# Performance work log

Measured on AMD Instinct MI355X. Metric: run time of the kernel, lower is better.

Reference implementation:

```python
import jax, jax.numpy as jnp
import numpy as np

T, N, E = 4, 50000, 800000
F, H, C_HID, C_OUT = 256, 128, 512, 2
SLOPE = 11.0 / 48.0  # torch RReLU eval-mode slope = (1/8 + 1/3) / 2


def _topk_pool(x, scorer, k):
    # x: [N, d], scorer: [d, 1] -> [d, k]
    scores = (x @ scorer) / jnp.maximum(jnp.linalg.norm(scorer), 1e-6)  # [N, 1]
    _, idx = jax.lax.top_k(scores[:, 0], k)
    return (x[idx] * jnp.tanh(scores[idx])).T


def _gru_cell(prev_Q, z, Wu, Uu, bu, Wr, Ur, br, Wh, Uh, bh):
    u = jax.nn.sigmoid(Wu @ z + Uu @ prev_Q + bu)
    r = jax.nn.sigmoid(Wr @ z + Ur @ prev_Q + br)
    h_cap = jnp.tanh(Wh @ z + Uh @ (r * prev_Q) + bh)
    return (1.0 - u) * prev_Q + u * h_cap


def _gcn_conv(x, src, dst, W):
    ones = jnp.ones(src.shape[0], x.dtype)
    deg_out = jnp.clip(jax.ops.segment_sum(ones, src, num_segments=N), 1.0)
    deg_in = jnp.clip(jax.ops.segment_sum(ones, dst, num_segments=N), 1.0)
    h = (x * (deg_out ** -0.5)[:, None]) @ W          # project first (out <= in)
    agg = jax.ops.segment_sum(h[src], dst, num_segments=N)
    out = agg * (deg_in ** -0.5)[:, None]
    return jnp.where(out >= 0, out, SLOPE * out)      # RReLU (eval mode)


def setup_inputs() -> dict:
    key = jax.random.key(0)
    ks = jax.random.split(key, 32)
    s = 0.05
    d = {}
    d['feats'] = jax.random.normal(ks[0], (T, N, F), jnp.float32)
    d['edges'] = jax.random.randint(ks[1], (T, 2, E), 0, N)
    d['scorer0'] = jax.random.normal(ks[2], (F, 1), jnp.float32) * s
    d['scorer1'] = jax.random.normal(ks[3], (H, 1), jnp.float32) * s
    d['gcn_W0'] = jax.random.normal(ks[4], (F, H), jnp.float32) * s
    d['gcn_W1'] = jax.random.normal(ks[5], (H, H), jnp.float32) * s
    i = 6
    for g in ('u', 'r', 'h'):
        d[g + '_W0'] = jax.random.normal(ks[i], (F, F), jnp.float32) * s; i += 1
        d[g + '_U0'] = jax.random.normal(ks[i], (F, F), jnp.float32) * s; i += 1
        d[g + '_b0'] = jax.random.normal(ks[i], (F, H), jnp.float32) * s; i += 1
    for g in ('u', 'r', 'h'):
        d[g + '_W1'] = jax.random.normal(ks[i], (H, H), jnp.float32) * s; i += 1
        d[g + '_U1'] = jax.random.normal(ks[i], (H, H), jnp.float32) * s; i += 1
        d[g + '_b1'] = jax.random.normal(ks[i], (H, H), jnp.float32) * s; i += 1
    d['mlp_W1'] = jax.random.normal(ks[i], (H, C_HID), jnp.float32) * s; i += 1
    d['mlp_b1'] = jax.random.normal(ks[i], (C_HID,), jnp.float32) * s; i += 1
    d['mlp_W2'] = jax.random.normal(ks[i], (C_HID, C_OUT), jnp.float32) * s; i += 1
    d['mlp_b2'] = jax.random.normal(ks[i], (C_OUT,), jnp.float32) * s
    return d


def reference(feats, edges, scorer0, scorer1, gcn_W0, gcn_W1,
              u_W0, u_U0, u_b0, r_W0, r_U0, r_b0, h_W0, h_U0, h_b0,
              u_W1, u_U1, u_b1, r_W1, r_U1, r_b1, h_W1, h_U1, h_b1,
              mlp_W1, mlp_b1, mlp_W2, mlp_b2):
    feat_list = [feats[t] for t in range(T)]
    scorers = [scorer0, scorer1]
    gcn_Ws = [gcn_W0, gcn_W1]
    grus = [(u_W0, u_U0, u_b0, r_W0, r_U0, r_b0, h_W0, h_U0, h_b0),
            (u_W1, u_U1, u_b1, r_W1, r_U1, r_b1, h_W1, h_U1, h_b1)]
    for i in range(2):
        W = gcn_Ws[i]
        for t in range(T):
            src, dst = edges[t, 0], edges[t, 1]
            X_tilde = _topk_pool(feat_list[t], scorers[i], H)
            W = _gru_cell(W, X_tilde, *grus[i])
            feat_list[t] = _gcn_conv(feat_list[t], src, dst, W)
    x = feat_list[-1]
    x = jnp.maximum(x @ mlp_W1 + mlp_b1, 0.0)
    return x @ mlp_W2 + mlp_b2
```

## Files before the change

### kernel.cpp

```cpp
#include <hip/hip_runtime.h>

#define NT 4
#define NN 50000
#define NE 800000
#define FD 256
#define HD 128
#define CH 512
#define NBINS 4096
#define CAPC 256
#define RSLOPE 0.22916666666666666f

#define NCH 32
#define CHE (NE / NCH)
#define HALFN 25000
#define WPH 12500
#define WPC 25000

#define C_NORM0 0
#define C_NORM1 1

#define SCAN_BLOCKS 49
#define BT0SZ (HD * 2 * FD)
#define BT1SZ (HD * 2 * HD)

#define SU_NORM0 0
#define SU_NORM1 1
#define SU_CVT_A 2
#define SU_CVT_B 66
#define SU_CVT_C 98
#define SU_CAT0 114
#define SU_CAT1 1650
#define SU_SPL0 2034
#define SU_SPL1 2290
#define SU_CPQ0 2354
#define SU_CPQ1 2386
#define SU_ZBAR 2402
#define SU_TOTAL 2403

typedef __attribute__((ext_vector_type(8))) short bf16x8;
typedef __attribute__((ext_vector_type(4))) float f32x4;

__device__ __forceinline__ float wsumf(float v) {
  for (int m = 32; m > 0; m >>= 1) v += __shfl_xor(v, m, 64);
  return v;
}

__device__ __forceinline__ unsigned short f2bf(float x) {
  unsigned int u = __float_as_uint(x);
  u += 0x7fffu + ((u >> 16) & 1u);
  return (unsigned short)(u >> 16);
}
__device__ __forceinline__ float bf2f(unsigned short h) {
  return __uint_as_float(((unsigned int)h) << 16);
}
__device__ __forceinline__ int sbin(float s) {
  int b = (int)floorf((s + 16.f) * 128.f);
  return max(0, min(NBINS - 1, b));
}

__device__ __forceinline__ void gbar(unsigned int* bar, int nblk, int gen) {
  __syncthreads();
  if (threadIdx.x == 0) {
    __threadfence();
    atomicAdd(bar, 1u);
    unsigned int tgt = (unsigned int)(nblk * (gen + 1));
    while (atomicAdd(bar, 0u) < tgt) __builtin_amdgcn_s_sleep(2);
    __threadfence();
  }
  __syncthreads();
}

__device__ __forceinline__ void d_norm(const float* s, int d, float* ctlf, int slot,
                                       float* red) {
  float v = ((int)threadIdx.x < d) ? s[threadIdx.x] * s[threadIdx.x] : 0.f;
  red[threadIdx.x] = v;
  __syncthreads();
  for (int o = 128; o > 0; o >>= 1) {
    if ((int)threadIdx.x < o) red[threadIdx.x] += red[threadIdx.x + o];
    __syncthreads();
  }
  if (threadIdx.x == 0) ctlf[slot] = fmaxf(sqrtf(red[0]), 1e-6f);
}

__device__ __forceinline__ void d_cvtT(int bx, int by, const float* __restrict__ src, int C,
                                       unsigned short* __restrict__ dhi,
                                       unsigned short* __restrict__ dlo,
                                       int ldd, int roff, float (*t)[33]) {
  int bc = bx * 32, br = by * 32;
  int lr = threadIdx.x >> 5, lc = threadIdx.x & 31;
#pragma unroll
  for (int q = 0; q < 4; ++q) {
    int r = br + lr + q * 8;
    t[lr + q * 8][lc] = src[(size_t)r * C + bc + lc];
  }
  __syncthreads();
#pragma unroll
  for (int q = 0; q < 4; ++q) {
    int dr = lr + q * 8;
    float v = t[lc][dr];
    unsigned short h = f2bf(v);
    unsigned short l = f2bf(v - bf2f(h));
    size_t o = (size_t)(bc + dr) * ldd + roff + br + lc;
    dhi[o] = h;
    dlo[o] = l;
  }
}

__device__ __forceinline__ void d_catsplit(int blk, int d, const float* __restrict__ Wu,
                                           const float* __restrict__ Uu,
                                           const float* __restrict__ Wr,
                                           const float* __restrict__ Ur,
                                           const float* __restrict__ Wh,
                                           unsigned short* __restrict__ hi,
                                           unsigned short* __restrict__ lo) {
  int idx = blk * 256 + threadIdx.x;
  int K = 2 * d;
  if (idx >= 3 * d * K) return;
  int row = idx / K, col = idx - row * K;
  int reg = row / d;
  int i = row - reg * d;
  float v;
  if (reg == 0) v = (col < d) ? Wu[i * d + col] : Uu[i * d + col - d];
  else if (reg == 1) v = (col < d) ? Wr[i * d + col] : Ur[i * d + col - d];
  else v = (col < d) ? Wh[i * d + col] : 0.f;
  unsigned short h = f2bf(v);
  hi[idx] = h;
  lo[idx] = f2bf(v - bf2f(h));
}

__device__ __forceinline__ void d_split(int blk, int n, const float* __restrict__ src,
                                        unsigned short* __restrict__ hi,
                                        unsigned short* __restrict__ lo) {
  int idx = blk * 256 + threadIdx.x;
  if (idx >= n) return;
  float v = src[idx];
  unsigned short h = f2bf(v);
  hi[idx] = h;
  lo[idx] = f2bf(v - bf2f(h));
}

__global__ __launch_bounds__(256) void k_startup(
    const float* __restrict__ scorer0, const float* __restrict__ scorer1,
    float* __restrict__ ctlf,
    const float* __restrict__ mlpW1, unsigned short* __restrict__ mW1thi,
    unsigned short* __restrict__ mW1tlo,
    const float* __restrict__ gcnW0, const float* __restrict__ gcnW1,
    unsigned short* __restrict__ bt0hi, unsigned short* __restrict__ bt0lo,
    unsigned short* __restrict__ bt1hi, unsigned short* __restrict__ bt1lo,
    const float* __restrict__ u_W0, const float* __restrict__ u_U0,
    const float* __restrict__ r_W0, const float* __restrict__ r_U0,
    const float* __restrict__ h_W0,
    unsigned short* __restrict__ acat0hi, unsigned short* __restrict__ acat0lo,
    const float* __restrict__ u_W1, const float* __restrict__ u_U1,
    const float* __restrict__ r_W1, const float* __restrict__ r_U1,
    const float* __restrict__ h_W1,
    unsigned short* __restrict__ acat1hi, unsigned short* __restrict__ acat1lo,
    const float* __restrict__ uh0, unsigned short* __restrict__ uh0hi,
    unsigned short* __restrict__ uh0lo,
    const float* __restrict__ uh1, unsigned short* __restrict__ uh1hi,
    unsigned short* __restrict__ uh1lo,
    float* __restrict__ Q0, float* __restrict__ Q1,
    unsigned int* __restrict__ bar) {
  __shared__ float red[256];
  __shared__ float tile[32][33];
  int b = blockIdx.x;
  if (b == SU_NORM0) { d_norm(scorer0, FD, ctlf, C_NORM0, red); return; }
  if (b == SU_NORM1) { d_norm(scorer1, HD, ctlf, C_NORM1, red); return; }
  if (b < SU_CVT_B) { int r = b - SU_CVT_A; d_cvtT(r & 15, r >> 4, mlpW1, CH, mW1thi, mW1tlo, HD, 0, tile); return; }
  if (b < SU_CVT_C) { int r = b - SU_CVT_B; d_cvtT(r & 3, r >> 2, gcnW0, HD, bt0hi, bt0lo, 2 * FD, FD, tile); return; }
  if (b < SU_CAT0)  { int r = b - SU_CVT_C; d_cvtT(r & 3, r >> 2, gcnW1, HD, bt1hi, bt1lo, 2 * HD, HD, tile); return; }
  if (b < SU_CAT1)  { d_catsplit(b - SU_CAT0, FD, u_W0, u_U0, r_W0, r_U0, h_W0, acat0hi, acat0lo); return; }
  if (b < SU_SPL0)  { d_catsplit(b - SU_CAT1, HD, u_W1, u_U1, r_W1, r_U1, h_W1, acat1hi, acat1lo); return; }
  if (b < SU_SPL1)  { d_split(b - SU_SPL0, FD * FD, uh0, uh0hi, uh0lo); return; }
  if (b < SU_CPQ0)  { d_split(b - SU_SPL1, HD * HD, uh1, uh1hi, uh1lo); return; }
  if (b < SU_CPQ1)  { int i = (b - SU_CPQ0) * 256 + threadIdx.x; ((float4*)Q0)[i] = ((const float4*)gcnW0)[i]; return; }
  if (b < SU_ZBAR)  { int i = (b - SU_CPQ1) * 256 + threadIdx.x; ((float4*)Q1)[i] = ((const float4*)gcnW1)[i]; return; }
  if (threadIdx.x < 16) bar[threadIdx.x] = 0;
}

__global__ __launch_bounds__(1024) void k_degC(const int* __restrict__ edges,
                                               unsigned int* __restrict__ chist) {
  __shared__ unsigned int lcnt[WPH];
  int t = blockIdx.y, c = blockIdx.x;
  int tid = threadIdx.x;
  for (int dir = 0; dir < 2; ++dir) {
    const int* E = edges + (size_t)t * 2 * NE + (size_t)dir * NE + (size_t)c * CHE;
    for (int half = 0; half < 2; ++half) {
      for (int i = tid; i < WPH; i += 1024) lcnt[i] = 0;
      __syncthreads();
      int lo = half * HALFN;
      for (int j = tid; j < CHE; j += 1024) {
        int n = E[j] - lo;
        if ((unsigned)n < (unsigned)HALFN)
          atomicAdd(&lcnt[n >> 1], 1u << ((n & 1) * 16));
      }
      __syncthreads();
      unsigned int* dst = chist + (((size_t)dir * NT + t) * NCH + c) * WPC + (size_t)half * WPH;
      for (int i = tid; i < WPH; i += 1024) dst[i] = lcnt[i];
      __syncthreads();
    }
  }
}

__global__ __launch_bounds__(1024) void k_scanB(const unsigned int* __restrict__ chist,
                                                unsigned int* __restrict__ lbase,
                                                float* __restrict__ dor4,
                                                float* __restrict__ din4,
                                                int* __restrict__ rowptr4,
                                                int* __restrict__ bsum4) {
  int t = blockIdx.y;
  int tid = threadIdx.x;
  int g = blockIdx.x * 1024 + tid;
  int lane = tid & 63, wid = tid >> 6;
  int v = 0;
  if (g < NN) {
    int w = g >> 1, sh = (g & 1) * 16;
    const unsigned int* oh = chist + ((size_t)0 * NT + t) * NCH * WPC;
    const unsigned int* ih = chist + ((size_t)1 * NT + t) * NCH * WPC;
    int o = 0;
#pragma unroll
    for (int c = 0; c < NCH; ++c) o += (oh[(size_t)c * WPC + w] >> sh) & 0xffff;
    dor4[t * NN + g] = 1.f / sqrtf((float)max(o, 1));
    int run = 0;
#pragma unroll
    for (int c = 0; c < NCH; ++c) {
      lbase[((size_t)t * NCH + c) * NN + g] = (unsigned int)run;
      run += (ih[(size_t)c * WPC + w] >> sh) & 0xffff;
    }
    v = run;
    din4[t * NN + g] = 1.f / sqrtf((float)max(v, 1));
  }
  int s = v;
  for (int o = 1; o < 64; o <<= 1) {
    int u = __shfl_up(s, o, 64);
    if (lane >= o) s += u;
  }
  __shared__ int ws[16];
  if (lane == 63) ws[wid] = s;
  __syncthreads();
  if (wid == 0 && lane < 16) {
    int u = ws[lane];
    int ss = u;
    for (int o = 1; o < 16; o <<= 1) {
      int w2 = __shfl_up(ss, o, 64);
      if (lane >= o) ss += w2;
    }
    ws[lane] = ss - u;
  }
  __syncthreads();
  int incl = s + ws[wid];
  if (g < NN) rowptr4[(size_t)t * (NN + 1) + g] = incl - v;
  if (tid == 1023) bsum4[t * SCAN_BLOCKS + blockIdx.x] = incl;
}

__global__ __launch_bounds__(1024) void k_scan2b(int* __restrict__ rowptr4,
                                                 const int* __restrict__ bsum4) {
  int t = blockIdx.x;
  int* rowptr = rowptr4 + (size_t)t * (NN + 1);
  const int* bsum = bsum4 + t * SCAN_BLOCKS;
  __shared__ int boff[SCAN_BLOCKS];
// ... 77 lines not shown
  __shared__ float stv[HD];
  __shared__ int sidx[HD];
  __shared__ int thrBin, cnt;
  int tid = threadIdx.x;
  for (int i = tid; i < NBINS; i += 1024) hist[i] = 0;
  if (tid == 0) cnt = 0;
  __syncthreads();
  for (int i = tid; i < NN; i += 1024) atomicAdd(&hist[sbin(scores[i])], 1);
  __syncthreads();

  int h0 = hist[4 * tid + 0], h1 = hist[4 * tid + 1];
  int h2 = hist[4 * tid + 2], h3 = hist[4 * tid + 3];
  int l3 = h3, l2 = h2 + l3, l1 = h1 + l2, l0 = h0 + l1;
  sufT[tid] = l0;
  __syncthreads();
  for (int off = 1; off < 1024; off <<= 1) {
    int u = (tid + off < 1024) ? sufT[tid + off] : 0;
    __syncthreads();
    sufT[tid] += u;
    __syncthreads();
  }
  {
    int higher = sufT[tid] - l0;
    int S0 = l0 + higher, S1 = l1 + higher, S2 = l2 + higher, S3 = l3 + higher;
    int S4 = higher;
    if (S3 >= HD && S4 < HD) thrBin = 4 * tid + 3;
    else if (S2 >= HD && S3 < HD) thrBin = 4 * tid + 2;
    else if (S1 >= HD && S2 < HD) thrBin = 4 * tid + 1;
    else if (S0 >= HD && S1 < HD) thrBin = 4 * tid + 0;
  }
  __syncthreads();
  int thr = thrBin;
  for (int i = tid; i < NN; i += 1024) {
    float s = scores[i];
    if (sbin(s) >= thr) {
      int p = atomicAdd(&cnt, 1);
      if (p < CAPC) { cs[p] = s; ci[p] = i; }
    }
  }
  __syncthreads();
  int M = min(cnt, CAPC);
  for (int i = tid; i < CAPC; i += 1024)
    if (i >= M) { cs[i] = -3.4e38f; ci[i] = 0x7fffffff; }
  __syncthreads();
  for (int k = 2; k <= CAPC; k <<= 1) {
    for (int j = k >> 1; j > 0; j >>= 1) {
      int i = tid;
      if (i < CAPC) {
        int l = i ^ j;
        if (l > i) {
          float si = cs[i], sl = cs[l];
          int di = ci[i], dl = ci[l];
          bool lb = (sl > si) || (sl == si && dl < di);
          bool ib = (si > sl) || (si == sl && di < dl);
          bool dir = ((i & k) == 0);
          if (dir ? lb : ib) {
            cs[i] = sl; cs[l] = si; ci[i] = dl; ci[l] = di;
          }
        }
      }
      __syncthreads();
    }
  }
  if (tid < HD) {
    stv[tid] = tanhf(cs[tid]);
    sidx[tid] = ci[tid];
  }
  __syncthreads();
  for (int e4 = tid * 4; e4 < D * HD; e4 += 1024 * 4) {
    int j = e4 >> LOGD, f = e4 & (D - 1);
    float4 x = *(const float4*)&X[(size_t)sidx[j] * D + f];
    float sv = stv[j];
    x.x *= sv; x.y *= sv; x.z *= sv; x.w *= sv;
    ushort4 h, l;
    h.x = f2bf(x.x); l.x = f2bf(x.x - bf2f(h.x));
    h.y = f2bf(x.y); l.y = f2bf(x.y - bf2f(h.y));
    h.z = f2bf(x.z); l.z = f2bf(x.z - bf2f(h.z));
    h.w = f2bf(x.w); l.w = f2bf(x.w - bf2f(h.w));
    *(ushort4*)&bthi[(size_t)j * ldb + f] = h;
    *(ushort4*)&btlo[(size_t)j * ldb + f] = l;
  }
}

__device__ __forceinline__ void gruA_body(
    int bx, const unsigned short* __restrict__ Ahi, const unsigned short* __restrict__ Alo,
    const unsigned short* __restrict__ Bhi, const unsigned short* __restrict__ Blo,
    int d, const float* __restrict__ bu, const float* __restrict__ br,
    const float* __restrict__ bh, const float* __restrict__ Q,
    float* __restrict__ u, float* __restrict__ hz,
    unsigned short* __restrict__ rqThi, unsigned short* __restrict__ rqTlo,
    unsigned short* AshH, unsigned short* AshL,
    unsigned short* BshH, unsigned short* BshL) {
  int K = 2 * d;
  int tid = threadIdx.x;
  int lane = tid & 63, wave = tid >> 6;
  int wr = wave >> 1, wc = wave & 1;
  int n0 = bx * 64;
  f32x4 acc[2][4];
#pragma unroll
  for (int m = 0; m < 2; ++m)
#pragma unroll
    for (int n = 0; n < 4; ++n) acc[m][n] = (f32x4){0.f, 0.f, 0.f, 0.f};
  int arow = tid >> 2, aseg = tid & 3;
  int as = (aseg ^ (arow & 3)) * 8;
  int kseg = lane >> 4;
  for (int k0 = 0; k0 < K; k0 += 32) {
    __syncthreads();
    {
      size_t off = (size_t)(n0 + arow) * K + k0 + aseg * 8;
      *(bf16x8*)&AshH[arow * 32 + as] = *(const bf16x8*)(Ahi + off);
      *(bf16x8*)&AshL[arow * 32 + as] = *(const bf16x8*)(Alo + off);
    }
#pragma unroll
    for (int h = 0; h < 2; ++h) {
      int id = tid + h * 256;
      int br2 = id >> 2, bseg = id & 3;
      int bs = (bseg ^ (br2 & 3)) * 8;
      size_t off = (size_t)br2 * K + k0 + bseg * 8;
      *(bf16x8*)&BshH[br2 * 32 + bs] = *(const bf16x8*)(Bhi + off);
      *(bf16x8*)&BshL[br2 * 32 + bs] = *(const bf16x8*)(Blo + off);
    }
    __syncthreads();
    bf16x8 ah[2], al[2], bh8[4], bl8[4];
#pragma unroll
    for (int m = 0; m < 2; ++m) {
      int row = wr * 32 + m * 16 + (lane & 15);
      int s = (kseg ^ (row & 3)) * 8;
      ah[m] = *(bf16x8*)&AshH[row * 32 + s];
      al[m] = *(bf16x8*)&AshL[row * 32 + s];
    }
#pragma unroll
    for (int n = 0; n < 4; ++n) {
      int col = wc * 64 + n * 16 + (lane & 15);
      int s = (kseg ^ (col & 3)) * 8;
      bh8[n] = *(bf16x8*)&BshH[col * 32 + s];
      bl8[n] = *(bf16x8*)&BshL[col * 32 + s];
    }
#pragma unroll
    for (int m = 0; m < 2; ++m)
#pragma unroll
      for (int n = 0; n < 4; ++n) {
        acc[m][n] = __builtin_amdgcn_mfma_f32_16x16x32_bf16(ah[m], bh8[n], acc[m][n], 0, 0, 0);
        acc[m][n] = __builtin_amdgcn_mfma_f32_16x16x32_bf16(al[m], bh8[n], acc[m][n], 0, 0, 0);
        acc[m][n] = __builtin_amdgcn_mfma_f32_16x16x32_bf16(ah[m], bl8[n], acc[m][n], 0, 0, 0);
      }
  }
  int reg = n0 / d;
#pragma unroll
  for (int m = 0; m < 2; ++m) {
#pragma unroll
    for (int q = 0; q < 4; ++q) {
      int row = n0 + wr * 32 + m * 16 + (lane >> 4) * 4 + q;
      int i = row - reg * d;
#pragma unroll
      for (int n = 0; n < 4; ++n) {
        int col = wc * 64 + n * 16 + (lane & 15);
        float a = acc[m][n][q];
        if (reg == 0) {
          u[i * HD + col] = 1.f / (1.f + expf(-(a + bu[i * HD + col])));
        } else if (reg == 1) {
          float r = 1.f / (1.f + expf(-(a + br[i * HD + col])));
          float rq = r * Q[i * HD + col];
          unsigned short h = f2bf(rq);
          rqThi[(size_t)col * d + i] = h;
          rqTlo[(size_t)col * d + i] = f2bf(rq - bf2f(h));
        } else {
          hz[i * HD + col] = a + bh[i * HD + col];
        }
      }
    }
  }
}

__device__ __forceinline__ void gruB_body(
    int bx, const unsigned short* __restrict__ Ahi, const unsigned short* __restrict__ Alo,
    const unsigned short* __restrict__ Bhi, const unsigned short* __restrict__ Blo,
    int d, const float* __restrict__ hz, const float* __restrict__ u,
    float* __restrict__ Q, unsigned short* __restrict__ BTWhi,
    unsigned short* __restrict__ BTWlo, int ldbt,
    unsigned short* AshH, unsigned short* AshL,
    unsigned short* BshH, unsigned short* BshL) {
  int K = d;
  int tid = threadIdx.x;
  int lane = tid & 63, wave = tid >> 6;
  int wr = wave >> 1, wc = wave & 1;
  int n0 = bx * 64;
  f32x4 acc[2][4];
#pragma unroll
  for (int m = 0; m < 2; ++m)
#pragma unroll
    for (int n = 0; n < 4; ++n) acc[m][n] = (f32x4){0.f, 0.f, 0.f, 0.f};
  int arow = tid >> 2, aseg = tid & 3;
  int as = (aseg ^ (arow & 3)) * 8;
  int kseg = lane >> 4;
  for (int k0 = 0; k0 < K; k0 += 32) {
    __syncthreads();
    {
      size_t off = (size_t)(n0 + arow) * K + k0 + aseg * 8;
      *(bf16x8*)&AshH[arow * 32 + as] = *(const bf16x8*)(Ahi + off);
      *(bf16x8*)&AshL[arow * 32 + as] = *(const bf16x8*)(Alo + off);
    }
#pragma unroll
    for (int h = 0; h < 2; ++h) {
      int id = tid + h * 256;
      int br2 = id >> 2, bseg = id & 3;
      int bs = (bseg ^ (br2 & 3)) * 8;
      size_t off = (size_t)br2 * K + k0 + bseg * 8;
      *(bf16x8*)&BshH[br2 * 32 + bs] = *(const bf16x8*)(Bhi + off);
      *(bf16x8*)&BshL[br2 * 32 + bs] = *(const bf16x8*)(Blo + off);
    }
    __syncthreads();
    bf16x8 ah[2], al[2], bh8[4], bl8[4];
#pragma unroll
    for (int m = 0; m < 2; ++m) {
      int row = wr * 32 + m * 16 + (lane & 15);
      int s = (kseg ^ (row & 3)) * 8;
      ah[m] = *(bf16x8*)&AshH[row * 32 + s];
      al[m] = *(bf16x8*)&AshL[row * 32 + s];
    }
#pragma unroll
    for (int n = 0; n < 4; ++n) {
      int col = wc * 64 + n * 16 + (lane & 15);
      int s = (kseg ^ (col & 3)) * 8;
      bh8[n] = *(bf16x8*)&BshH[col * 32 + s];
      bl8[n] = *(bf16x8*)&BshL[col * 32 + s];
    }
#pragma unroll
    for (int m = 0; m < 2; ++m)
#pragma unroll
      for (int n = 0; n < 4; ++n) {
        acc[m][n] = __builtin_amdgcn_mfma_f32_16x16x32_bf16(ah[m], bh8[n], acc[m][n], 0, 0, 0);
        acc[m][n] = __builtin_amdgcn_mfma_f32_16x16x32_bf16(al[m], bh8[n], acc[m][n], 0, 0, 0);
        acc[m][n] = __builtin_amdgcn_mfma_f32_16x16x32_bf16(ah[m], bl8[n], acc[m][n], 0, 0, 0);
      }
  }
#pragma unroll
  for (int m = 0; m < 2; ++m) {
#pragma unroll
    for (int q = 0; q < 4; ++q) {
      int i = n0 + wr * 32 + m * 16 + (lane >> 4) * 4 + q;
#pragma unroll
      for (int n = 0; n < 4; ++n) {
        int col = wc * 64 + n * 16 + (lane & 15);
        float hc = tanhf(acc[m][n][q] + hz[i * HD + col]);
        float uu = u[i * HD + col];
        float qv = Q[i * HD + col];
        float wn = (1.f - uu) * qv + uu * hc;
        Q[i * HD + col] = wn;
        unsigned short h = f2bf(wn);
        BTWhi[(size_t)col * ldbt + i] = h;
        BTWlo[(size_t)col * ldbt + i] = f2bf(wn - bf2f(h));
      }
    }
  }
}

__global__ __launch_bounds__(256) void k_gruChain(
    const unsigned short* __restrict__ Ahi, const unsigned short* __restrict__ Alo,
    unsigned short* __restrict__ bthi, unsigned short* __restrict__ btlo, long btSz,
    int d, const float* __restrict__ gb_u, const float* __restrict__ gb_r,
    const float* __restrict__ gb_h, float* __restrict__ Q,
    float* __restrict__ ubuf, float* __restrict__ hzbuf,
    unsigned short* __restrict__ rqThi, unsigned short* __restrict__ rqTlo,
    const unsigned short* __restrict__ uhhi, const unsigned short* __restrict__ uhlo,
    unsigned int* bar) {
  __shared__ unsigned short AshH[64 * 32], AshL[64 * 32];
  __shared__ unsigned short BshH[128 * 32], BshL[128 * 32];
  int nb = (int)gridDim.x;
  for (int t = 0; t < NT; ++t) {
    gruA_body((int)blockIdx.x, Ahi, Alo,
              bthi + (size_t)t * btSz, btlo + (size_t)t * btSz, d,
              gb_u, gb_r, gb_h, Q, ubuf, hzbuf, rqThi, rqTlo,
              AshH, AshL, BshH, BshL);
    gbar(bar, nb, 2 * t);
    if ((int)blockIdx.x < (d >> 6)) {
      size_t nxt = (size_t)((t + 1) & 3) * btSz;
      gruB_body((int)blockIdx.x, uhhi, uhlo, rqThi, rqTlo, d, hzbuf, ubuf, Q,
                bthi + nxt + d, btlo + nxt + d, 2 * d,
                AshH, AshL, BshH, BshL);
    }
    if (t < NT - 1) gbar(bar, nb, 2 * t + 1);
  }
}

__global__ __launch_bounds__(256) void k_convL0(
    const float* __restrict__ feats,
    const unsigned short* __restrict__ bt0hi, const unsigned short* __restrict__ bt0lo,
    float* __restrict__ C4, const float* __restrict__ dor4) {
  __shared__ unsigned short AshH[64 * 32], AshL[64 * 32];
  __shared__ unsigned short BshH[128 * 32], BshL[128 * 32];
  const int K = FD, ldb = 2 * FD;
  int t = blockIdx.z;
  const float* Af = feats + (size_t)t * NN * FD;
  size_t bOff = (size_t)((t + 1) & 3) * BT0SZ + FD;
  const unsigned short* Bhi = bt0hi + bOff;
  const unsigned short* Blo = bt0lo + bOff;
  float* C = C4 + (size_t)t * NN * HD;
  const float* rs = dor4 + (size_t)t * NN;
  int tid = threadIdx.x;
  int lane = tid & 63, wave = tid >> 6;
  int wr = wave >> 1, wc = wave & 1;
  int n0 = blockIdx.x * 64;
  f32x4 acc[2][4];
#pragma unroll
  for (int m = 0; m < 2; ++m)
#pragma unroll
    for (int n = 0; n < 4; ++n) acc[m][n] = (f32x4){0.f, 0.f, 0.f, 0.f};

  int arow = tid >> 2, aseg = tid & 3;
  int as = (aseg ^ (arow & 3)) * 8;
  int kseg = lane >> 4;

  for (int k0 = 0; k0 < K; k0 += 32) {
    __syncthreads();
    {
      bf16x8 vh = (bf16x8)(short)0, vl = (bf16x8)(short)0;
      int row = n0 + arow;
      if (row < NN) {
        const float* g = Af + (size_t)row * K + k0 + aseg * 8;
        float4 v0 = *(const float4*)g;
        float4 v1 = *(const float4*)(g + 4);
        float xs[8] = {v0.x, v0.y, v0.z, v0.w, v1.x, v1.y, v1.z, v1.w};
#pragma unroll
        for (int j = 0; j < 8; ++j) {
          unsigned short h = f2bf(xs[j]);
          vh[j] = (short)h;
          vl[j] = (short)f2bf(xs[j] - bf2f(h));
        }
      }
      *(bf16x8*)&AshH[arow * 32 + as] = vh;
      *(bf16x8*)&AshL[arow * 32 + as] = vl;
    }
#pragma unroll
    for (int h = 0; h < 2; ++h) {
      int id = tid + h * 256;
      int br = id >> 2, bseg = id & 3;
      int bs = (bseg ^ (br & 3)) * 8;
      size_t off = (size_t)br * ldb + k0 + bseg * 8;
      *(bf16x8*)&BshH[br * 32 + bs] = *(const bf16x8*)(Bhi + off);
      *(bf16x8*)&BshL[br * 32 + bs] = *(const bf16x8*)(Blo + off);
    }
    __syncthreads();

    bf16x8 ah[2], al[2], bh[4], bl[4];
#pragma unroll
    for (int m = 0; m < 2; ++m) {
      int row = wr * 32 + m * 16 + (lane & 15);
      int s = (kseg ^ (row & 3)) * 8;
      ah[m] = *(bf16x8*)&AshH[row * 32 + s];
      al[m] = *(bf16x8*)&AshL[row * 32 + s];
    }
#pragma unroll
    for (int n = 0; n < 4; ++n) {
      int col = wc * 64 + n * 16 + (lane & 15);
      int s = (kseg ^ (col & 3)) * 8;
      bh[n] = *(bf16x8*)&BshH[col * 32 + s];
      bl[n] = *(bf16x8*)&BshL[col * 32 + s];
    }
#pragma unroll
    for (int m = 0; m < 2; ++m)
#pragma unroll
      for (int n = 0; n < 4; ++n) {
        acc[m][n] = __builtin_amdgcn_mfma_f32_16x16x32_bf16(ah[m], bh[n], acc[m][n], 0, 0, 0);
        acc[m][n] = __builtin_amdgcn_mfma_f32_16x16x32_bf16(al[m], bh[n], acc[m][n], 0, 0, 0);
// ... 174 lines not shown
#pragma unroll
    for (int m = 0; m < 2; ++m)
#pragma unroll
      for (int n = 0; n < 4; ++n) acc[m][n] = (f32x4){0.f, 0.f, 0.f, 0.f};
    for (int k0 = 0; k0 < HD; k0 += 32) {
      __syncthreads();
#pragma unroll
      for (int h2 = 0; h2 < 2; ++h2) {
        int id = tid + h2 * 256;
        int br = id >> 2, bseg = id & 3;
        int bs = (bseg ^ (br & 3)) * 8;
        size_t off = (size_t)(hc * 128 + br) * HD + k0 + bseg * 8;
        *(bf16x8*)&BshH[br * 32 + bs] = *(const bf16x8*)(Bhi + off);
        *(bf16x8*)&BshL[br * 32 + bs] = *(const bf16x8*)(Blo + off);
      }
      __syncthreads();
      bf16x8 ah[2], al[2], bh[4], bl[4];
#pragma unroll
      for (int m = 0; m < 2; ++m) {
        int row = wr * 32 + m * 16 + (lane & 15);
        int sg = (k0 >> 3) + kseg;
        int sp = (sg ^ (row & 15)) * 8;
        ah[m] = *(bf16x8*)&AshH[row * 128 + sp];
        al[m] = *(bf16x8*)&AshL[row * 128 + sp];
      }
#pragma unroll
      for (int n = 0; n < 4; ++n) {
        int col = wc * 64 + n * 16 + (lane & 15);
        int s = (kseg ^ (col & 3)) * 8;
        bh[n] = *(bf16x8*)&BshH[col * 32 + s];
        bl[n] = *(bf16x8*)&BshL[col * 32 + s];
      }
#pragma unroll
      for (int m = 0; m < 2; ++m)
#pragma unroll
        for (int n = 0; n < 4; ++n) {
          acc[m][n] = __builtin_amdgcn_mfma_f32_16x16x32_bf16(ah[m], bh[n], acc[m][n], 0, 0, 0);
          acc[m][n] = __builtin_amdgcn_mfma_f32_16x16x32_bf16(al[m], bh[n], acc[m][n], 0, 0, 0);
          acc[m][n] = __builtin_amdgcn_mfma_f32_16x16x32_bf16(ah[m], bl[n], acc[m][n], 0, 0, 0);
        }
    }
#pragma unroll
    for (int n = 0; n < 4; ++n) {
      int col = hc * 128 + wc * 64 + n * 16 + (lane & 15);
      float bcol = bias[col];
      float w20 = W2[2 * col], w21 = W2[2 * col + 1];
#pragma unroll
      for (int m = 0; m < 2; ++m)
#pragma unroll
        for (int q = 0; q < 4; ++q) {
          float v = fmaxf(acc[m][n][q] + bcol, 0.f);
          ps0[m][q] += v * w20;
          ps1[m][q] += v * w21;
        }
    }
  }
#pragma unroll
  for (int m = 0; m < 2; ++m)
#pragma unroll
    for (int q = 0; q < 4; ++q) {
      float a = ps0[m][q], b = ps1[m][q];
      for (int msk = 8; msk > 0; msk >>= 1) {
        a += __shfl_xor(a, msk, 64);
        b += __shfl_xor(b, msk, 64);
      }
      if ((lane & 15) == 0) {
        int r = wr * 32 + m * 16 + (lane >> 4) * 4 + q;
        atomicAdd(&osum[r][0], a);
        atomicAdd(&osum[r][1], b);
      }
    }
  __syncthreads();
  if (tid < 64) {
    int row = n0 + tid;
    if (row < M) {
      out[(size_t)row * 2 + 0] = osum[tid][0] + b2[0];
      out[(size_t)row * 2 + 1] = osum[tid][1] + b2[1];
    }
  }
}

__global__ void k_aggB(const float* __restrict__ h4, const int* __restrict__ rowptr4,
                       const int* __restrict__ srcs4, const float* __restrict__ din4,
                       float* __restrict__ featA4, const float* __restrict__ scorer,
                       const float* __restrict__ ctlf, float* __restrict__ scores1_4,
                       unsigned short* __restrict__ outHi, unsigned short* __restrict__ outLo) {
  int t = blockIdx.y;
  int w = (blockIdx.x * blockDim.x + threadIdx.x) >> 6;
  int lane = threadIdx.x & 63;
  if (w >= NN) return;
  const float* h = h4 + (size_t)t * NN * HD;
  const int* rowptr = rowptr4 + (size_t)t * (NN + 1);
  const int* srcs = srcs4 + (size_t)t * NE;
  int beg = rowptr[w], end = rowptr[w + 1];
  float ax = 0.f, ay = 0.f;
  int e = beg;
  int l2o = lane * 2;
  for (; e + 8 <= end; e += 8) {
    int s0 = srcs[e + 0], s1 = srcs[e + 1], s2 = srcs[e + 2], s3 = srcs[e + 3];
    int s4 = srcs[e + 4], s5 = srcs[e + 5], s6 = srcs[e + 6], s7 = srcs[e + 7];
    float2 v0 = *(const float2*)&h[(size_t)s0 * HD + l2o];
    float2 v1 = *(const float2*)&h[(size_t)s1 * HD + l2o];
    float2 v2 = *(const float2*)&h[(size_t)s2 * HD + l2o];
    float2 v3 = *(const float2*)&h[(size_t)s3 * HD + l2o];
    float2 v4 = *(const float2*)&h[(size_t)s4 * HD + l2o];
    float2 v5 = *(const float2*)&h[(size_t)s5 * HD + l2o];
    float2 v6 = *(const float2*)&h[(size_t)s6 * HD + l2o];
    float2 v7 = *(const float2*)&h[(size_t)s7 * HD + l2o];
    ax += ((v0.x + v1.x) + (v2.x + v3.x)) + ((v4.x + v5.x) + (v6.x + v7.x));
    ay += ((v0.y + v1.y) + (v2.y + v3.y)) + ((v4.y + v5.y) + (v6.y + v7.y));
  }
  for (; e + 2 <= end; e += 2) {
    int s0 = srcs[e + 0], s1 = srcs[e + 1];
    float2 v0 = *(const float2*)&h[(size_t)s0 * HD + l2o];
    float2 v1 = *(const float2*)&h[(size_t)s1 * HD + l2o];
    ax += v0.x + v1.x;
    ay += v0.y + v1.y;
  }
  for (; e < end; ++e) {
    int s = srcs[e];
    float2 v = *(const float2*)&h[(size_t)s * HD + l2o];
    ax += v.x; ay += v.y;
  }
  float dn = din4[(size_t)t * NN + w];
  ax *= dn; ay *= dn;
  ax = ax >= 0.f ? ax : RSLOPE * ax;
  ay = ay >= 0.f ? ay : RSLOPE * ay;
  *(float2*)&featA4[((size_t)t * NN + w) * HD + l2o] = make_float2(ax, ay);
  if (t == NT - 1) {
    unsigned short hx = f2bf(ax), hy = f2bf(ay);
    unsigned short lx = f2bf(ax - bf2f(hx)), ly = f2bf(ay - bf2f(hy));
    *(ushort2*)&outHi[(size_t)w * HD + l2o] = make_ushort2(hx, hy);
    *(ushort2*)&outLo[(size_t)w * HD + l2o] = make_ushort2(lx, ly);
  }
  float sp = ax * scorer[l2o] + ay * scorer[l2o + 1];
  sp = wsumf(sp);
  if (lane == 0) scores1_4[(size_t)t * NN + w] = sp / ctlf[C_NORM1];
}

extern "C" void kernel_launch(void* const* d_in, const int* in_sizes, int n_in,
                              void* d_out, int out_size, void* d_ws, size_t ws_size,
                              hipStream_t stream) {
  (void)in_sizes; (void)n_in; (void)out_size; (void)ws_size;
  const float* feats = (const float*)d_in[0];
  const int* edges = (const int*)d_in[1];
  const float* scorer0 = (const float*)d_in[2];
  const float* scorer1 = (const float*)d_in[3];
  const float* gcnW0 = (const float*)d_in[4];
  const float* gcnW1 = (const float*)d_in[5];
  const float* g0[9];
  const float* g1[9];
  for (int i = 0; i < 9; ++i) {
    g0[i] = (const float*)d_in[6 + i];
    g1[i] = (const float*)d_in[15 + i];
  }
  const float* mlpW1 = (const float*)d_in[24];
  const float* mlpB1 = (const float*)d_in[25];
  const float* mlpW2 = (const float*)d_in[26];
  const float* mlpB2 = (const float*)d_in[27];
  float* out = (float*)d_out;

  char* p = (char*)d_ws;
  auto carve = [&p](size_t bytes) {
    void* r = (void*)p;
    p += (bytes + 511) & ~(size_t)511;
    return r;
  };
  float* featA4 = (float*)carve((size_t)NT * NN * HD * 4);
  float* hbuf4  = (float*)carve((size_t)NT * NN * HD * 4);
  unsigned short* fahi = (unsigned short*)carve((size_t)NN * HD * 2);
  unsigned short* falo = (unsigned short*)carve((size_t)NN * HD * 2);
  int* srcs4   = (int*)carve((size_t)NT * NE * 4);
  int* rowptr4 = (int*)carve((size_t)NT * (NN + 1) * 4);
  unsigned int* chist = (unsigned int*)carve((size_t)2 * NT * NCH * WPC * 4);
  unsigned int* lbase = (unsigned int*)carve((size_t)NT * NCH * NN * 4);
  int* bsum4   = (int*)carve((size_t)NT * SCAN_BLOCKS * 4);
  float* dor4  = (float*)carve((size_t)NT * NN * 4);
  float* din4  = (float*)carve((size_t)NT * NN * 4);
  float* scores0 = (float*)carve((size_t)NT * NN * 4);
  float* scores1_4 = (float*)carve((size_t)NT * NN * 4);
  float* ctlf  = (float*)carve(64 * 4);
  unsigned short* bt0hi = (unsigned short*)carve((size_t)NT * BT0SZ * 2);
  unsigned short* bt0lo = (unsigned short*)carve((size_t)NT * BT0SZ * 2);
  unsigned short* bt1hi = (unsigned short*)carve((size_t)NT * BT1SZ * 2);
  unsigned short* bt1lo = (unsigned short*)carve((size_t)NT * BT1SZ * 2);
  unsigned short* rqThi = (unsigned short*)carve((size_t)HD * FD * 2);
  unsigned short* rqTlo = (unsigned short*)carve((size_t)HD * FD * 2);
  float* ubuf_f = (float*)carve((size_t)FD * HD * 4);
  float* hzbuf  = (float*)carve((size_t)FD * HD * 4);
  unsigned short* acat0hi = (unsigned short*)carve((size_t)3 * FD * 2 * FD * 2);
  unsigned short* acat0lo = (unsigned short*)carve((size_t)3 * FD * 2 * FD * 2);
  unsigned short* acat1hi = (unsigned short*)carve((size_t)3 * HD * 2 * HD * 2);
  unsigned short* acat1lo = (unsigned short*)carve((size_t)3 * HD * 2 * HD * 2);
  unsigned short* uh0hi = (unsigned short*)carve((size_t)FD * FD * 2);
  unsigned short* uh0lo = (unsigned short*)carve((size_t)FD * FD * 2);
  unsigned short* uh1hi = (unsigned short*)carve((size_t)HD * HD * 2);
  unsigned short* uh1lo = (unsigned short*)carve((size_t)HD * HD * 2);
  float* Q0 = (float*)carve((size_t)FD * HD * 4);
  float* Q1 = (float*)carve((size_t)HD * HD * 4);
  unsigned short* mW1thi = (unsigned short*)carve((size_t)CH * HD * 2);
  unsigned short* mW1tlo = (unsigned short*)carve((size_t)CH * HD * 2);
  unsigned int* barbuf = (unsigned int*)carve(64 * 4);

  k_startup<<<SU_TOTAL, 256, 0, stream>>>(
      scorer0, scorer1, ctlf, mlpW1, mW1thi, mW1tlo, gcnW0, gcnW1,
      bt0hi, bt0lo, bt1hi, bt1lo,
      g0[0], g0[1], g0[3], g0[4], g0[6], acat0hi, acat0lo,
      g1[0], g1[1], g1[3], g1[4], g1[6], acat1hi, acat1lo,
      g0[7], uh0hi, uh0lo, g1[7], uh1hi, uh1lo, Q0, Q1, barbuf);

  k_scores0_all<<<dim3(12500, NT), 256, 0, stream>>>(feats, scorer0, ctlf, scores0);
  k_degC<<<dim3(NCH, NT), 1024, 0, stream>>>(edges, chist);
  k_scanB<<<dim3(SCAN_BLOCKS, NT), 1024, 0, stream>>>(chist, lbase, dor4, din4, rowptr4, bsum4);
  k_scan2b<<<NT, 1024, 0, stream>>>(rowptr4, bsum4);
  k_scatC<<<dim3(NCH, NT), 1024, 0, stream>>>(edges, rowptr4, lbase, srcs4);
  k_pool<8><<<NT, 1024, 0, stream>>>(feats, (long)NN * FD, scores0, NN,
                                     bt0hi, bt0lo, (long)BT0SZ, 2 * FD);

  k_gruChain<<<3 * FD / 64, 256, 0, stream>>>(
      acat0hi, acat0lo, bt0hi, bt0lo, (long)BT0SZ, FD,
      g0[2], g0[5], g0[8], Q0, ubuf_f, hzbuf, rqThi, rqTlo,
      uh0hi, uh0lo, barbuf + 0);

  const int gM = (NN + 63) / 64;

  k_convL0<<<dim3(gM, 1, NT), 256, 0, stream>>>(feats, bt0hi, bt0lo, hbuf4, dor4);

  k_aggB<<<dim3(12500, NT), 256, 0, stream>>>(hbuf4, rowptr4, srcs4, din4, featA4,
                                              scorer1, ctlf, scores1_4, fahi, falo);

  k_pool<7><<<NT, 1024, 0, stream>>>(featA4, (long)NN * HD, scores1_4, NN,
                                     bt1hi, bt1lo, (long)BT1SZ, 2 * HD);

  k_gruChain<<<3 * HD / 64, 256, 0, stream>>>(
      acat1hi, acat1lo, bt1hi, bt1lo, (long)BT1SZ, HD,
      g1[2], g1[5], g1[8], Q1, ubuf_f, hzbuf, rqThi, rqTlo,
      uh1hi, uh1lo, barbuf + 1);

  k_gemm3<<<dim3(gM, 1), 256, 0, stream>>>(fahi, falo, HD,
                                           bt1hi + HD, bt1lo + HD, 2 * HD,
                                           hbuf4, HD, NN, HD, dor4 + (size_t)3 * NN);
  k_gemmMLPagg<<<gM, 256, 0, stream>>>(hbuf4, rowptr4 + (size_t)3 * (NN + 1),
                                       srcs4 + (size_t)3 * NE, din4 + (size_t)3 * NN,
                                       mW1thi, mW1tlo, mlpB1, mlpW2, mlpB2, out, NN);
}
```

Measured before the change: 1.126 ms.

## Drop featA buffer by recomputing pooled rows; split GRU chain into per-step launches

The layer-1 aggregation no longer writes the full fp32 featA tensor (4x50000x128). A new pool kernel instead recomputes aggregation, normalization and RReLU only for the 128 selected top-k nodes, directly from hbuf and the CSR. The persistent GRU chain kernel with its spin-wait grid barriers is replaced by separate gruA/gruB launches for each timestep. This removes a large write and reread of intermediate data and the barrier spinning, at the cost of 16 extra kernel launches and some redundant gather work in the pool kernel.

```diff
diff --git a/kernel.cpp b/kernel.cpp
--- a/kernel.cpp
+++ b/kernel.cpp
@@ -34,8 +34,7 @@
 #define SU_SPL1 2290
 #define SU_CPQ0 2354
 #define SU_CPQ1 2386
-#define SU_ZBAR 2402
-#define SU_TOTAL 2403
+#define SU_TOTAL 2402
 
 typedef __attribute__((ext_vector_type(8))) short bf16x8;
 typedef __attribute__((ext_vector_type(4))) float f32x4;
@@ -56,18 +55,6 @@
 __device__ __forceinline__ int sbin(float s) {
   int b = (int)floorf((s + 16.f) * 128.f);
   return max(0, min(NBINS - 1, b));
-}
-
-__device__ __forceinline__ void gbar(unsigned int* bar, int nblk, int gen) {
-  __syncthreads();
-  if (threadIdx.x == 0) {
-    __threadfence();
-    atomicAdd(bar, 1u);
-    unsigned int tgt = (unsigned int)(nblk * (gen + 1));
-    while (atomicAdd(bar, 0u) < tgt) __builtin_amdgcn_s_sleep(2);
-    __threadfence();
-  }
-  __syncthreads();
 }
 
 __device__ __forceinline__ void d_norm(const float* s, int d, float* ctlf, int slot,
@@ -159,8 +146,7 @@
     unsigned short* __restrict__ uh0lo,
     const float* __restrict__ uh1, unsigned short* __restrict__ uh1hi,
     unsigned short* __restrict__ uh1lo,
-    float* __restrict__ Q0, float* __restrict__ Q1,
-    unsigned int* __restrict__ bar) {
+    float* __restrict__ Q0, float* __restrict__ Q1) {
   __shared__ float red[256];
   __shared__ float tile[32][33];
   int b = blockIdx.x;
@@ -174,8 +160,7 @@
   if (b < SU_SPL1)  { d_split(b - SU_SPL0, FD * FD, uh0, uh0hi, uh0lo); return; }
   if (b < SU_CPQ0)  { d_split(b - SU_SPL1, HD * HD, uh1, uh1hi, uh1lo); return; }
   if (b < SU_CPQ1)  { int i = (b - SU_CPQ0) * 256 + threadIdx.x; ((float4*)Q0)[i] = ((const float4*)gcnW0)[i]; return; }
-  if (b < SU_ZBAR)  { int i = (b - SU_CPQ1) * 256 + threadIdx.x; ((float4*)Q1)[i] = ((const float4*)gcnW1)[i]; return; }
-  if (threadIdx.x < 16) bar[threadIdx.x] = 0;
+  { int i = (b - SU_CPQ1) * 256 + threadIdx.x; ((float4*)Q1)[i] = ((const float4*)gcnW1)[i]; }
 }
 
 __global__ __launch_bounds__(1024) void k_degC(const int* __restrict__ edges,
@@ -419,20 +404,20 @@
   }
 }
 
-__device__ __forceinline__ void gruA_body(
-    int bx, const unsigned short* __restrict__ Ahi, const unsigned short* __restrict__ Alo,
+__global__ __launch_bounds__(256) void k_gruA(
+    const unsigned short* __restrict__ Ahi, const unsigned short* __restrict__ Alo,
     const unsigned short* __restrict__ Bhi, const unsigned short* __restrict__ Blo,
     int d, const float* __restrict__ bu, const float* __restrict__ br,
     const float* __restrict__ bh, const float* __restrict__ Q,
     float* __restrict__ u, float* __restrict__ hz,
-    unsigned short* __restrict__ rqThi, unsigned short* __restrict__ rqTlo,
-    unsigned short* AshH, unsigned short* AshL,
-    unsigned short* BshH, unsigned short* BshL) {
+    unsigned short* __restrict__ rqThi, unsigned short* __restrict__ rqTlo) {
+  __shared__ unsigned short AshH[64 * 32], AshL[64 * 32];
+  __shared__ unsigned short BshH[128 * 32], BshL[128 * 32];
   int K = 2 * d;
   int tid = threadIdx.x;
   int lane = tid & 63, wave = tid >> 6;
   int wr = wave >> 1, wc = wave & 1;
-  int n0 = bx * 64;
+  int n0 = blockIdx.x * 64;
   f32x4 acc[2][4];
 #pragma unroll
   for (int m = 0; m < 2; ++m)
@@ -509,19 +494,19 @@
   }
 }
 
-__device__ __forceinline__ void gruB_body(
-    int bx, const unsigned short* __restrict__ Ahi, const unsigned short* __restrict__ Alo,
+__global__ __launch_bounds__(256) void k_gruB(
+    const unsigned short* __restrict__ Ahi, const unsigned short* __restrict__ Alo,
     const unsigned short* __restrict__ Bhi, const unsigned short* __restrict__ Blo,
     int d, const float* __restrict__ hz, const float* __restrict__ u,
     float* __restrict__ Q, unsigned short* __restrict__ BTWhi,
-    unsigned short* __restrict__ BTWlo, int ldbt,
-    unsigned short* AshH, unsigned short* AshL,
-    unsigned short* BshH, unsigned short* BshL) {
+    unsigned short* __restrict__ BTWlo, int ldbt) {
+  __shared__ unsigned short AshH[64 * 32], AshL[64 * 32];
+  __shared__ unsigned short BshH[128 * 32], BshL[128 * 32];
   int K = d;
   int tid = threadIdx.x;
   int lane = tid & 63, wave = tid >> 6;
   int wr = wave >> 1, wc = wave & 1;
-  int n0 = bx * 64;
+  int n0 = blockIdx.x * 64;
   f32x4 acc[2][4];
 #pragma unroll
   for (int m = 0; m < 2; ++m)
@@ -589,34 +574,6 @@
         BTWlo[(size_t)col * ldbt + i] = f2bf(wn - bf2f(h));
       }
     }
-  }
-}
-
-__global__ __launch_bounds__(256) void k_gruChain(
-    const unsigned short* __restrict__ Ahi, const unsigned short* __restrict__ Alo,
-    unsigned short* __restrict__ bthi, unsigned short* __restrict__ btlo, long btSz,
-    int d, const float* __restrict__ gb_u, const float* __restrict__ gb_r,
-    const float* __restrict__ gb_h, float* __restrict__ Q,
-    float* __restrict__ ubuf, float* __restrict__ hzbuf,
-    unsigned short* __restrict__ rqThi, unsigned short* __restrict__ rqTlo,
-    const unsigned short* __restrict__ uhhi, const unsigned short* __restrict__ uhlo,
-    unsigned int* bar) {
-  __shared__ unsigned short AshH[64 * 32], AshL[64 * 32];
-  __shared__ unsigned short BshH[128 * 32], BshL[128 * 32];
-  int nb = (int)gridDim.x;
-  for (int t = 0; t < NT; ++t) {
-    gruA_body((int)blockIdx.x, Ahi, Alo,
-              bthi + (size_t)t * btSz, btlo + (size_t)t * btSz, d,
-              gb_u, gb_r, gb_h, Q, ubuf, hzbuf, rqThi, rqTlo,
-              AshH, AshL, BshH, BshL);
-    gbar(bar, nb, 2 * t);
-    if ((int)blockIdx.x < (d >> 6)) {
-      size_t nxt = (size_t)((t + 1) & 3) * btSz;
-      gruB_body((int)blockIdx.x, uhhi, uhlo, rqThi, rqTlo, d, hzbuf, ubuf, Q,
-                bthi + nxt + d, btlo + nxt + d, 2 * d,
-                AshH, AshL, BshH, BshL);
-    }
-    if (t < NT - 1) gbar(bar, nb, 2 * t + 1);
   }
 }
 
@@ -957,7 +914,7 @@
 
 __global__ void k_aggB(const float* __restrict__ h4, const int* __restrict__ rowptr4,
                        const int* __restrict__ srcs4, const float* __restrict__ din4,
-                       float* __restrict__ featA4, const float* __restrict__ scorer,
+                       const float* __restrict__ scorer,
                        const float* __restrict__ ctlf, float* __restrict__ scores1_4,
                        unsigned short* __restrict__ outHi, unsigned short* __restrict__ outLo) {
   int t = blockIdx.y;
@@ -1001,7 +958,6 @@
   ax *= dn; ay *= dn;
   ax = ax >= 0.f ? ax : RSLOPE * ax;
   ay = ay >= 0.f ? ay : RSLOPE * ay;
-  *(float2*)&featA4[((size_t)t * NN + w) * HD + l2o] = make_float2(ax, ay);
   if (t == NT - 1) {
     unsigned short hx = f2bf(ax), hy = f2bf(ay);
     unsigned short lx = f2bf(ax - bf2f(hx)), ly = f2bf(ay - bf2f(hy));
@@ -1011,6 +967,116 @@
   float sp = ax * scorer[l2o] + ay * scorer[l2o + 1];
   sp = wsumf(sp);
   if (lane == 0) scores1_4[(size_t)t * NN + w] = sp / ctlf[C_NORM1];
+}
+
+__global__ __launch_bounds__(1024) void k_pool1(const float* __restrict__ hbuf4,
+                                                const int* __restrict__ rowptr4,
+                                                const int* __restrict__ srcs4,
+                                                const float* __restrict__ din4,
+                                                const float* __restrict__ scores1_4,
+                                                unsigned short* __restrict__ bt1hi,
+                                                unsigned short* __restrict__ bt1lo) {
+  int t = blockIdx.x;
+  const float* scores = scores1_4 + (size_t)t * NN;
+  const float* h = hbuf4 + (size_t)t * NN * HD;
+  const int* rowptr = rowptr4 + (size_t)t * (NN + 1);
+  const int* srcs = srcs4 + (size_t)t * NE;
+  const float* din = din4 + (size_t)t * NN;
+  unsigned short* bthi = bt1hi + (size_t)t * BT1SZ;
+  unsigned short* btlo = bt1lo + (size_t)t * BT1SZ;
+  __shared__ int hist[NBINS];
+  __shared__ int sufT[1024];
+  __shared__ float cs[CAPC];
+  __shared__ int ci[CAPC];
+  __shared__ float stv[HD];
+  __shared__ int sidx[HD];
+  __shared__ int thrBin, cnt;
+  int tid = threadIdx.x;
+  for (int i = tid; i < NBINS; i += 1024) hist[i] = 0;
+  if (tid == 0) cnt = 0;
+  __syncthreads();
+  for (int i = tid; i < NN; i += 1024) atomicAdd(&hist[sbin(scores[i])], 1);
+  __syncthreads();
+
+  int h0 = hist[4 * tid + 0], h1 = hist[4 * tid + 1];
+  int h2 = hist[4 * tid + 2], h3 = hist[4 * tid + 3];
+  int l3 = h3, l2 = h2 + l3, l1 = h1 + l2, l0 = h0 + l1;
+  sufT[tid] = l0;
+  __syncthreads();
+  for (int off = 1; off < 1024; off <<= 1) {
+    int u = (tid + off < 1024) ? sufT[tid + off] : 0;
+    __syncthreads();
+    sufT[tid] += u;
+    __syncthreads();
+  }
+  {
+    int higher = sufT[tid] - l0;
+    int S0 = l0 + higher, S1 = l1 + higher, S2 = l2 + higher, S3 = l3 + higher;
+    int S4 = higher;
+    if (S3 >= HD && S4 < HD) thrBin = 4 * tid + 3;
+    else if (S2 >= HD && S3 < HD) thrBin = 4 * tid + 2;
+    else if (S1 >= HD && S2 < HD) thrBin = 4 * tid + 1;
+    else if (S0 >= HD && S1 < HD) thrBin = 4 * tid + 0;
+  }
+  __syncthreads();
+  int thr = thrBin;
+  for (int i = tid; i < NN; i += 1024) {
+    float s = scores[i];
+    if (sbin(s) >= thr) {
+      int p = atomicAdd(&cnt, 1);
+      if (p < CAPC) { cs[p] = s; ci[p] = i; }
+    }
+  }
+  __syncthreads();
+  int M = min(cnt, CAPC);
+  for (int i = tid; i < CAPC; i += 1024)
+    if (i >= M) { cs[i] = -3.4e38f; ci[i] = 0x7fffffff; }
+  __syncthreads();
+  for (int k = 2; k <= CAPC; k <<= 1) {
+    for (int j = k >> 1; j > 0; j >>= 1) {
+      int i = tid;
+      if (i < CAPC) {
+        int l = i ^ j;
+        if (l > i) {
+          float si = cs[i], sl = cs[l];
+          int di = ci[i], dl = ci[l];
+          bool lb = (sl > si) || (sl == si && dl < di);
+          bool ib = (si > sl) || (si == sl && di < dl);
+          bool dir = ((i & k) == 0);
+          if (dir ? lb : ib) {
+            cs[i] = sl; cs[l] = si; ci[i] = dl; ci[l] = di;
+          }
+        }
+      }
+      __syncthreads();
+    }
+  }
+  if (tid < HD) {
+    stv[tid] = tanhf(cs[tid]);
+    sidx[tid] = ci[tid];
+  }
+  __syncthreads();
+  int wid = tid >> 6, lane = tid & 63;
+  int l2o = lane * 2;
+  for (int j = wid; j < HD; j += 16) {
+    int id = sidx[j];
+    int beg = rowptr[id], end = rowptr[id + 1];
+    float ax = 0.f, ay = 0.f;
+    for (int e = beg; e < end; ++e) {
+      float2 vv = *(const float2*)&h[(size_t)srcs[e] * HD + l2o];
+      ax += vv.x; ay += vv.y;
+    }
+    float dn = din[id];
+    ax *= dn; ay *= dn;
+    ax = ax >= 0.f ? ax : RSLOPE * ax;
+    ay = ay >= 0.f ? ay : RSLOPE * ay;
+    float sv = stv[j];
+    ax *= sv; ay *= sv;
+    unsigned short hx = f2bf(ax), hy = f2bf(ay);
+    unsigned short lx = f2bf(ax - bf2f(hx)), ly = f2bf(ay - bf2f(hy));
+    *(ushort2*)&bthi[(size_t)j * (2 * HD) + l2o] = make_ushort2(hx, hy);
+    *(ushort2*)&btlo[(size_t)j * (2 * HD) + l2o] = make_ushort2(lx, ly);
+  }
 }
 
 extern "C" void kernel_launch(void* const* d_in, const int* in_sizes, int n_in,
@@ -1041,7 +1107,6 @@
     p += (bytes + 511) & ~(size_t)511;
     return r;
   };
-  float* featA4 = (float*)carve((size_t)NT * NN * HD * 4);
   float* hbuf4  = (float*)carve((size_t)NT * NN * HD * 4);
   unsigned short* fahi = (unsigned short*)carve((size_t)NN * HD * 2);
   unsigned short* falo = (unsigned short*)carve((size_t)NN * HD * 2);
@@ -1075,14 +1140,13 @@
   float* Q1 = (float*)carve((size_t)HD * HD * 4);
   unsigned short* mW1thi = (unsigned short*)carve((size_t)CH * HD * 2);
   unsigned short* mW1tlo = (unsigned short*)carve((size_t)CH * HD * 2);
-  unsigned int* barbuf = (unsigned int*)carve(64 * 4);
 
   k_startup<<<SU_TOTAL, 256, 0, stream>>>(
       scorer0, scorer1, ctlf, mlpW1, mW1thi, mW1tlo, gcnW0, gcnW1,
       bt0hi, bt0lo, bt1hi, bt1lo,
       g0[0], g0[1], g0[3], g0[4], g0[6], acat0hi, acat0lo,
       g1[0], g1[1], g1[3], g1[4], g1[6], acat1hi, acat1lo,
-      g0[7], uh0hi, uh0lo, g1[7], uh1hi, uh1lo, Q0, Q1, barbuf);
+      g0[7], uh0hi, uh0lo, g1[7], uh1hi, uh1lo, Q0, Q1);
 
   k_scores0_all<<<dim3(12500, NT), 256, 0, stream>>>(feats, scorer0, ctlf, scores0);
   k_degC<<<dim3(NCH, NT), 1024, 0, stream>>>(edges, chist);
@@ -1092,25 +1156,35 @@
   k_pool<8><<<NT, 1024, 0, stream>>>(feats, (long)NN * FD, scores0, NN,
                                      bt0hi, bt0lo, (long)BT0SZ, 2 * FD);
 
-  k_gruChain<<<3 * FD / 64, 256, 0, stream>>>(
-      acat0hi, acat0lo, bt0hi, bt0lo, (long)BT0SZ, FD,
-      g0[2], g0[5], g0[8], Q0, ubuf_f, hzbuf, rqThi, rqTlo,
-      uh0hi, uh0lo, barbuf + 0);
+  for (int t = 0; t < NT; ++t) {
+    size_t btOff = (size_t)t * BT0SZ;
+    size_t btNxt = (size_t)((t + 1) & 3) * BT0SZ;
+    k_gruA<<<3 * FD / 64, 256, 0, stream>>>(acat0hi, acat0lo, bt0hi + btOff, bt0lo + btOff,
+                                            FD, g0[2], g0[5], g0[8], Q0, ubuf_f, hzbuf,
+                                            rqThi, rqTlo);
+    k_gruB<<<FD / 64, 256, 0, stream>>>(uh0hi, uh0lo, rqThi, rqTlo, FD, hzbuf, ubuf_f, Q0,
+                                        bt0hi + btNxt + FD, bt0lo + btNxt + FD, 2 * FD);
+  }
 
   const int gM = (NN + 63) / 64;
 
   k_convL0<<<dim3(gM, 1, NT), 256, 0, stream>>>(feats, bt0hi, bt0lo, hbuf4, dor4);
 
-  k_aggB<<<dim3(12500, NT), 256, 0, stream>>>(hbuf4, rowptr4, srcs4, din4, featA4,
+  k_aggB<<<dim3(12500, NT), 256, 0, stream>>>(hbuf4, rowptr4, srcs4, din4,
                                               scorer1, ctlf, scores1_4, fahi, falo);
 
-  k_pool<7><<<NT, 1024, 0, stream>>>(featA4, (long)NN * HD, scores1_4, NN,
-                                     bt1hi, bt1lo, (long)BT1SZ, 2 * HD);
-
-  k_gruChain<<<3 * HD / 64, 256, 0, stream>>>(
-      acat1hi, acat1lo, bt1hi, bt1lo, (long)BT1SZ, HD,
-      g1[2], g1[5], g1[8], Q1, ubuf_f, hzbuf, rqThi, rqTlo,
-      uh1hi, uh1lo, barbuf + 1);
+  k_pool1<<<NT, 1024, 0, stream>>>(hbuf4, rowptr4, srcs4, din4, scores1_4,
+                                   bt1hi, bt1lo);
+
+  for (int t = 0; t < NT; ++t) {
+    size_t btOff = (size_t)t * BT1SZ;
+    size_t btNxt = (size_t)((t + 1) & 3) * BT1SZ;
+    k_gruA<<<3 * HD / 64, 256, 0, stream>>>(acat1hi, acat1lo, bt1hi + btOff, bt1lo + btOff,
+                                            HD, g1[2], g1[5], g1[8], Q1, ubuf_f, hzbuf,
+                                            rqThi, rqTlo);
+    k_gruB<<<HD / 64, 256, 0, stream>>>(uh1hi, uh1lo, rqThi, rqTlo, HD, hzbuf, ubuf_f, Q1,
+                                        bt1hi + btNxt + HD, bt1lo + btNxt + HD, 2 * HD);
+  }
 
   k_gemm3<<<dim3(gM, 1), 256, 0, stream>>>(fahi, falo, HD,
                                            bt1hi + HD, bt1lo + HD, 2 * HD,
```

Result: slower. 1.152 ms (+2.4%).
